# Performance work log

Hardware: AMD Instinct MI355X
Metric: run time of the kernel (lower is better)

## Reference

```python
import jax, jax.numpy as jnp
import numpy as np
from jax import lax

T, B, I, H = 512, 32, 1024, 1024


def setup_inputs() -> dict:
    key = jax.random.key(0)
    ks = jax.random.split(key, 7)
    s_i = 1.0 / np.sqrt(I)
    s_h = 1.0 / np.sqrt(H)
    return {
        "x": jax.random.normal(ks[0], (T, B, I), jnp.float32),
        "w_ih_0": jax.random.normal(ks[1], (4 * H, I), jnp.float32) * s_i,
        "w_hh_0": jax.random.normal(ks[2], (4 * H, H), jnp.float32) * s_h,
        "b_0": jax.random.normal(ks[3], (4 * H,), jnp.float32) * 0.1,
        "w_ih_1": jax.random.normal(ks[4], (4 * H, H), jnp.float32) * s_h,
        "w_hh_1": jax.random.normal(ks[5], (4 * H, H), jnp.float32) * s_h,
        "b_1": jax.random.normal(ks[6], (4 * H,), jnp.float32) * 0.1,
    }


def _sublstm_layer(inp, w_ih, w_hh, b):
    # Premultiply all timesteps at once (PremulLayer): [T,B,4H]
    pre = jnp.einsum('tbi,gi->tbg', inp, w_ih) + b
    Bsz = inp.shape[1]
    Hd = w_hh.shape[1]
    w_hh_t = w_hh.T  # [H,4H]

    def step(carry, p_t):
        h, c = carry
        gates = jax.nn.sigmoid(p_t + h @ w_hh_t)  # [B,4H]
        i_g, o_g, z_g, f_g = jnp.split(gates, 4, axis=-1)
        c = c * f_g + z_g - i_g
        h = jax.nn.sigmoid(c) - o_g
        return (h, c), h

    init = (jnp.zeros((Bsz, Hd), inp.dtype), jnp.zeros((Bsz, Hd), inp.dtype))
    _, outs = lax.scan(step, init, pre)
    return outs  # [T,B,H]


def reference(x, w_ih_0, w_hh_0, b_0, w_ih_1, w_hh_1, b_1):
    out = _sublstm_layer(x, w_ih_0, w_hh_0, b_0)
    out = _sublstm_layer(out, w_ih_1, w_hh_1, b_1)
    return out
```

## Files before the change

### kernel.cpp

```cpp
#include <hip/hip_runtime.h>
#include <hip/hip_fp16.h>
#include <stdint.h>

typedef _Float16 f16;
typedef _Float16 f16x8 __attribute__((ext_vector_type(8)));
typedef _Float16 f16x4 __attribute__((ext_vector_type(4)));
typedef float f32x4 __attribute__((ext_vector_type(4)));
typedef unsigned u32x4 __attribute__((ext_vector_type(4)));

#define TSTEPS 512
#define NB 256
#define NT 512
#define HN (32 * 1024)

__device__ __forceinline__ float sigm(float v) { return 1.0f / (1.0f + __expf(-v)); }

__device__ __forceinline__ void ld_coh(f16x8& d, const f16* p) {
  asm volatile("global_load_dwordx4 %0, %1, off sc0 sc1" : "=v"(d) : "v"(p));
}
__device__ __forceinline__ void ld_plain(f16x8& d, const f16* p) {
  asm volatile("global_load_dwordx4 %0, %1, off" : "=v"(d) : "v"(p));
}
__device__ __forceinline__ void st_coh_f16(f16* p, f16 v) {
  asm volatile("global_store_short %0, %1, off sc0 sc1" :: "v"(p), "v"(v) : "memory");
}
__device__ __forceinline__ void st_coh_u32(unsigned* p, unsigned v) {
  asm volatile("global_store_dword %0, %1, off sc0 sc1" :: "v"(p), "v"(v) : "memory");
}
__device__ __forceinline__ u32x4 ld_coh_u4(const unsigned* p) {
  u32x4 d;
  asm volatile("global_load_dwordx4 %0, %1, off sc0 sc1" : "=v"(d) : "v"(p));
  return d;
}
__device__ __forceinline__ unsigned ld_coh_u32(const unsigned* p) {
  unsigned d;
  asm volatile("global_load_dword %0, %1, off sc0 sc1" : "=v"(d) : "v"(p));
  return d;
}

template<int USE_X16>
__global__ __launch_bounds__(NT, 2)
void sublstm_persistent(const float* __restrict__ x,
                        const float* __restrict__ wih0, const float* __restrict__ whh0,
                        const float* __restrict__ b0,
                        const float* __restrict__ wih1, const float* __restrict__ whh1,
                        const float* __restrict__ b1,
                        const f16* __restrict__ x16,
                        f16* __restrict__ h1buf, f16* __restrict__ h2buf,
                        unsigned* __restrict__ bar,
                        float* __restrict__ out)
{
  __shared__ float red[8][16][68];
  __shared__ float gatesS[16][68];
  __shared__ float biasS[64];

  const int bid   = blockIdx.x;
  const int layer = bid >> 7;
  const int n     = (bid & 127) >> 1;
  const int r     = bid & 1;
  const int tid   = threadIdx.x;
  const int lane  = tid & 63;
  const int w     = tid >> 6;
  const int c15   = lane & 15;
  const int g4    = lane >> 4;
  unsigned* genp  = bar + 320;

  const float* wih = layer ? wih1 : wih0;
  const float* whh = layer ? whh1 : whh0;
  const float* bb  = layer ? b1   : b0;

  const int kbase = w * 256 + g4 * 8;
  f16x8 breg[4][8];
  #pragma unroll
  for (int cc = 0; cc < 4; ++cc) {
    const int gate = cc * 1024 + (n << 4) + c15;
    const float* wr = (w < 4) ? (wih + (size_t)gate * 1024 + kbase)
                              : (whh + (size_t)gate * 1024 + (kbase - 1024));
    #pragma unroll
    for (int ks = 0; ks < 8; ++ks) {
      const float4 v0 = *(const float4*)(wr + ks * 32);
      const float4 v1 = *(const float4*)(wr + ks * 32 + 4);
      breg[cc][ks] = (f16x8){(f16)v0.x,(f16)v0.y,(f16)v0.z,(f16)v0.w,
                             (f16)v1.x,(f16)v1.y,(f16)v1.z,(f16)v1.w};
    }
  }
  if (tid < 64) biasS[tid] = bb[(tid >> 4) * 1024 + (n << 4) + (tid & 15)];
  __syncthreads();

  float c = 0.0f;
  f16x8 af[8];
  const int arow = r * 16 + c15;

  for (int s = 0; s <= TSTEPS; ++s) {
    const int p_in  = s & 1;
    const int p_out = (s + 1) & 1;
    const bool active = (layer == 0) ? (s < TSTEPS) : (s >= 1);
    const int t = (layer == 0) ? s : (s - 1);
    const unsigned us = (unsigned)s;

    if (active && layer == 0 && w < 4) {
      if (USE_X16) {
        const f16* bp = x16 + ((size_t)t * 32 + arow) * 1024 + kbase;
        #pragma unroll
        for (int ks = 0; ks < 8; ++ks) ld_plain(af[ks], bp + ks * 32);
      } else {
        const float* bp = x + ((size_t)t * 32 + arow) * 1024 + kbase;
        #pragma unroll
        for (int ks = 0; ks < 8; ++ks) {
          const float4 v0 = *(const float4*)(bp + ks * 32);
          const float4 v1 = *(const float4*)(bp + ks * 32 + 4);
          af[ks] = (f16x8){(f16)v0.x,(f16)v0.y,(f16)v0.z,(f16)v0.w,
                           (f16)v1.x,(f16)v1.y,(f16)v1.z,(f16)v1.w};
        }
      }
    }

    if (s >= 1) {
      if (bid == 0 && w == 0) {
        while (true) {
          u32x4 d = ld_coh_u4(bar + (lane << 2));
          asm volatile("s_waitcnt vmcnt(0)" ::: "memory");
          __builtin_amdgcn_sched_barrier(0);
          if (__all(d.x >= us && d.y >= us && d.z >= us && d.w >= us)) break;
          __builtin_amdgcn_s_sleep(1);
        }
        if (lane == 0) st_coh_u32(genp, us);
      } else if (tid == 0) {
        while (true) {
          const unsigned gv = ld_coh_u32(genp);
          asm volatile("s_waitcnt vmcnt(0)" ::: "memory");
          __builtin_amdgcn_sched_barrier(0);
          if (gv >= us) break;
          __builtin_amdgcn_s_sleep(1);
        }
      }
      __syncthreads();
    }

    if (active) {
      if (!(layer == 0 && w < 4)) {
        const f16* src; int koff;
        if (layer == 0)   { src = h1buf + (size_t)p_in * HN; koff = kbase - 1024; }
        else if (w < 4)   { src = h1buf + (size_t)p_in * HN; koff = kbase; }
        else              { src = h2buf + (size_t)p_in * HN; koff = kbase - 1024; }
        const f16* bp = src + (size_t)arow * 1024 + koff;
        #pragma unroll
        for (int ks = 0; ks < 8; ++ks) ld_coh(af[ks], bp + ks * 32);
      }
      asm volatile("s_waitcnt vmcnt(0)" ::: "memory");
      __builtin_amdgcn_sched_barrier(0);

      f32x4 acc[4] = {{0,0,0,0},{0,0,0,0},{0,0,0,0},{0,0,0,0}};
      #pragma unroll
      for (int ks = 0; ks < 8; ++ks)
        #pragma unroll
        for (int cc = 0; cc < 4; ++cc)
          acc[cc] = __builtin_amdgcn_mfma_f32_16x16x32_f16(af[ks], breg[cc][ks], acc[cc], 0, 0, 0);

      #pragma unroll
      for (int cc = 0; cc < 4; ++cc)
        #pragma unroll
        for (int rr = 0; rr < 4; ++rr)
          red[w][g4 * 4 + rr][cc * 16 + c15] = acc[cc][rr];
    }
    __syncthreads();

    if (active) {
      #pragma unroll
      for (int rep = 0; rep < 2; ++rep) {
        const int idx = tid + rep * 512;
        const int lb = idx >> 6, col = idx & 63;
        float tot = biasS[col];
        #pragma unroll
        for (int ww = 0; ww < 8; ++ww) tot += red[ww][lb][col];
        gatesS[lb][col] = sigm(tot);
      }
    }
    __syncthreads();

    if (active && tid < 256) {
      const int lb = tid >> 4, u = tid & 15;
      const float ig = gatesS[lb][u];
      const float og = gatesS[lb][16 + u];
      const float zg = gatesS[lb][32 + u];
      const float fg = gatesS[lb][48 + u];
      c = c * fg + zg - ig;
      const float h = sigm(c) - og;
      const int b = r * 16 + lb;
      const int j = (n << 4) + u;
      f16* hb = ((layer == 0) ? h1buf : h2buf) + (size_t)p_out * HN;
      st_coh_f16(hb + b * 1024 + j, (f16)h);
      if (layer == 1) out[((size_t)t * 32 + b) * 1024 + j] = h;
    }

    asm volatile("s_waitcnt vmcnt(0)" ::: "memory");
    __syncthreads();
    if (tid == 0 && s < TSTEPS) st_coh_u32(bar + bid, us + 1u);
  }
}

__global__ void cvt_x_kernel(const float4* __restrict__ in, f16x4* __restrict__ outv, int n4) {
  int i = blockIdx.x * blockDim.x + threadIdx.x;
  const int stride = gridDim.x * blockDim.x;
  for (; i < n4; i += stride) {
    const float4 v = in[i];
    outv[i] = (f16x4){(f16)v.x, (f16)v.y, (f16)v.z, (f16)v.w};
  }
}

extern "C" void kernel_launch(void* const* d_in, const int* in_sizes, int n_in,
                              void* d_out, int out_size, void* d_ws, size_t ws_size,
                              hipStream_t stream) {
  const float* x    = (const float*)d_in[0];
  const float* wih0 = (const float*)d_in[1];
  const float* whh0 = (const float*)d_in[2];
  const float* b0   = (const float*)d_in[3];
  const float* wih1 = (const float*)d_in[4];
  const float* whh1 = (const float*)d_in[5];
  const float* b1   = (const float*)d_in[6];
  float* out = (float*)d_out;

  const size_t X16B   = (size_t)512 * 32 * 1024 * 2;
  const size_t HBUFB  = (size_t)2 * HN * 2;
  const size_t STATEB = 2 * HBUFB + 4096;

  char* ws = (char*)d_ws;
  const bool use_x16 = ws_size >= X16B + STATEB;
  const size_t soff = use_x16 ? X16B : 0;
  f16* x16        = (f16*)ws;
  f16* h1buf      = (f16*)(ws + soff);
  f16* h2buf      = (f16*)(ws + soff + HBUFB);
  unsigned* bar   = (unsigned*)(ws + soff + 2 * HBUFB);

  (void)hipMemsetAsync(ws + soff, 0, STATEB, stream);

  if (use_x16) {
    const int n4 = 512 * 32 * 1024 / 4;
    cvt_x_kernel<<<2048, 256, 0, stream>>>((const float4*)x, (f16x4*)x16, n4);
    sublstm_persistent<1><<<NB, NT, 0, stream>>>(x, wih0, whh0, b0, wih1, whh1, b1,
                                                 x16, h1buf, h2buf, bar, out);
  } else {
    sublstm_persistent<0><<<NB, NT, 0, stream>>>(x, wih0, whh0, b0, wih1, whh1, b1,
                                                 x16, h1buf, h2buf, bar, out);
  }
}
```

Measured before the change: 2.455 ms.

## Pad barrier flags to separate cache lines and fan out generation flags

Each block's arrival flag now sits on its own 64-byte line, and the coordinator writes 64 separate generation flags. Blocks poll these in groups, so they no longer all spin on one shared line. The hidden-state loads now go through normal caching, with an acquire fence placed after the barrier. The output stores become coherent stores. Together this aims to cut contention and latency on the global grid barrier and the h loads. The risk is correctness if the acquire fence does not invalidate stale cached h data, and the coordinator now issues four scalar loads per lane instead of one vector load.

```diff
diff --git a/kernel.cpp b/kernel.cpp
--- a/kernel.cpp
+++ b/kernel.cpp
@@ -15,22 +15,17 @@
 
 __device__ __forceinline__ float sigm(float v) { return 1.0f / (1.0f + __expf(-v)); }
 
-__device__ __forceinline__ void ld_coh(f16x8& d, const f16* p) {
-  asm volatile("global_load_dwordx4 %0, %1, off sc0 sc1" : "=v"(d) : "v"(p));
-}
 __device__ __forceinline__ void ld_plain(f16x8& d, const f16* p) {
   asm volatile("global_load_dwordx4 %0, %1, off" : "=v"(d) : "v"(p));
 }
 __device__ __forceinline__ void st_coh_f16(f16* p, f16 v) {
   asm volatile("global_store_short %0, %1, off sc0 sc1" :: "v"(p), "v"(v) : "memory");
 }
+__device__ __forceinline__ void st_coh_f32(float* p, float v) {
+  asm volatile("global_store_dword %0, %1, off sc0 sc1" :: "v"(p), "v"(v) : "memory");
+}
 __device__ __forceinline__ void st_coh_u32(unsigned* p, unsigned v) {
   asm volatile("global_store_dword %0, %1, off sc0 sc1" :: "v"(p), "v"(v) : "memory");
-}
-__device__ __forceinline__ u32x4 ld_coh_u4(const unsigned* p) {
-  u32x4 d;
-  asm volatile("global_load_dwordx4 %0, %1, off sc0 sc1" : "=v"(d) : "v"(p));
-  return d;
 }
 __device__ __forceinline__ unsigned ld_coh_u32(const unsigned* p) {
   unsigned d;
@@ -63,7 +58,6 @@
   const int w     = tid >> 6;
   const int c15   = lane & 15;
   const int g4    = lane >> 4;
-  unsigned* genp  = bar + 320;
 
   const float* wih = layer ? wih1 : wih0;
   const float* whh = layer ? whh1 : whh0;
@@ -118,16 +112,20 @@
     if (s >= 1) {
       if (bid == 0 && w == 0) {
         while (true) {
-          u32x4 d = ld_coh_u4(bar + (lane << 2));
+          const unsigned f0 = ld_coh_u32(bar + (lane * 4 + 0) * 16);
+          const unsigned f1 = ld_coh_u32(bar + (lane * 4 + 1) * 16);
+          const unsigned f2 = ld_coh_u32(bar + (lane * 4 + 2) * 16);
+          const unsigned f3 = ld_coh_u32(bar + (lane * 4 + 3) * 16);
           asm volatile("s_waitcnt vmcnt(0)" ::: "memory");
           __builtin_amdgcn_sched_barrier(0);
-          if (__all(d.x >= us && d.y >= us && d.z >= us && d.w >= us)) break;
+          if (__all(f0 >= us && f1 >= us && f2 >= us && f3 >= us)) break;
           __builtin_amdgcn_s_sleep(1);
         }
-        if (lane == 0) st_coh_u32(genp, us);
+        st_coh_u32(bar + 4096 + lane * 16, us);
       } else if (tid == 0) {
+        const unsigned* gp = bar + 4096 + (bid & 63) * 16;
         while (true) {
-          const unsigned gv = ld_coh_u32(genp);
+          const unsigned gv = ld_coh_u32(gp);
           asm volatile("s_waitcnt vmcnt(0)" ::: "memory");
           __builtin_amdgcn_sched_barrier(0);
           if (gv >= us) break;
@@ -135,6 +133,7 @@
         }
       }
       __syncthreads();
+      __builtin_amdgcn_fence(__ATOMIC_ACQUIRE, "agent");
     }
 
     if (active) {
@@ -145,7 +144,7 @@
         else              { src = h2buf + (size_t)p_in * HN; koff = kbase - 1024; }
         const f16* bp = src + (size_t)arow * 1024 + koff;
         #pragma unroll
-        for (int ks = 0; ks < 8; ++ks) ld_coh(af[ks], bp + ks * 32);
+        for (int ks = 0; ks < 8; ++ks) ld_plain(af[ks], bp + ks * 32);
       }
       asm volatile("s_waitcnt vmcnt(0)" ::: "memory");
       __builtin_amdgcn_sched_barrier(0);
@@ -190,12 +189,12 @@
       const int j = (n << 4) + u;
       f16* hb = ((layer == 0) ? h1buf : h2buf) + (size_t)p_out * HN;
       st_coh_f16(hb + b * 1024 + j, (f16)h);
-      if (layer == 1) out[((size_t)t * 32 + b) * 1024 + j] = h;
+      if (layer == 1) st_coh_f32(out + ((size_t)t * 32 + b) * 1024 + j, h);
     }
 
     asm volatile("s_waitcnt vmcnt(0)" ::: "memory");
     __syncthreads();
-    if (tid == 0 && s < TSTEPS) st_coh_u32(bar + bid, us + 1u);
+    if (tid == 0 && s < TSTEPS) st_coh_u32(bar + bid * 16, us + 1u);
   }
 }
 
@@ -222,7 +221,8 @@
 
   const size_t X16B   = (size_t)512 * 32 * 1024 * 2;
   const size_t HBUFB  = (size_t)2 * HN * 2;
-  const size_t STATEB = 2 * HBUFB + 4096;
+  const size_t BARB   = 32768;
+  const size_t STATEB = 2 * HBUFB + BARB;
 
   char* ws = (char*)d_ws;
   const bool use_x16 = ws_size >= X16B + STATEB;
```

Measured after the change: 9.641 ms. +292.7%, slower.

## Tag hidden-state words with step counters to replace the global barrier wait

Applied to the files above, without the earlier changes.

Each hidden value is now stored as a 32-bit word holding the fp16 value plus a step tag in the upper half. Consumers spin on their own input slices until every tag matches the expected step, instead of waiting for the centralized generation barrier before loading. The remaining generation-barrier wait, which still guards against overwriting the double buffer, is moved after the gate computation. The goal is to take the global barrier round trip off the critical path. In exchange the hidden-state loads are twice as wide, each poll spins on several vector loads, and buffer reuse safety now depends on the later barrier.

```diff
diff --git a/kernel.cpp b/kernel.cpp
--- a/kernel.cpp
+++ b/kernel.cpp
@@ -15,14 +15,8 @@
 
 __device__ __forceinline__ float sigm(float v) { return 1.0f / (1.0f + __expf(-v)); }
 
-__device__ __forceinline__ void ld_coh(f16x8& d, const f16* p) {
-  asm volatile("global_load_dwordx4 %0, %1, off sc0 sc1" : "=v"(d) : "v"(p));
-}
 __device__ __forceinline__ void ld_plain(f16x8& d, const f16* p) {
   asm volatile("global_load_dwordx4 %0, %1, off" : "=v"(d) : "v"(p));
-}
-__device__ __forceinline__ void st_coh_f16(f16* p, f16 v) {
-  asm volatile("global_store_short %0, %1, off sc0 sc1" :: "v"(p), "v"(v) : "memory");
 }
 __device__ __forceinline__ void st_coh_u32(unsigned* p, unsigned v) {
   asm volatile("global_store_dword %0, %1, off sc0 sc1" :: "v"(p), "v"(v) : "memory");
@@ -46,7 +40,7 @@
                         const float* __restrict__ wih1, const float* __restrict__ whh1,
                         const float* __restrict__ b1,
                         const f16* __restrict__ x16,
-                        f16* __restrict__ h1buf, f16* __restrict__ h2buf,
+                        unsigned* __restrict__ h1u, unsigned* __restrict__ h2u,
                         unsigned* __restrict__ bar,
                         float* __restrict__ out)
 {
@@ -115,17 +109,85 @@
       }
     }
 
-    if (s >= 1) {
-      if (bid == 0 && w == 0) {
+    if (s >= 1 && bid == 0 && w == 0) {
+      while (true) {
+        u32x4 d = ld_coh_u4(bar + (lane << 2));
+        asm volatile("s_waitcnt vmcnt(0)" ::: "memory");
+        __builtin_amdgcn_sched_barrier(0);
+        if (__all(d.x >= us && d.y >= us && d.z >= us && d.w >= us)) break;
+        __builtin_amdgcn_s_sleep(1);
+      }
+      if (lane == 0) st_coh_u32(genp, us);
+    }
+
+    if (active) {
+      if (!(layer == 0 && w < 4)) {
+        const unsigned* srcU; int koff; unsigned expv;
+        if (layer == 0)   { srcU = h1u + (size_t)p_in * HN; koff = kbase - 1024; expv = us; }
+        else if (w < 4)   { srcU = h1u + (size_t)p_in * HN; koff = kbase;        expv = us; }
+        else              { srcU = h2u + (size_t)p_in * HN; koff = kbase - 1024; expv = (s == 1) ? 0u : us; }
+        const unsigned* bp = srcU + (size_t)arow * 1024 + koff;
+        const unsigned expw = expv << 16;
+        u32x4 t0[8], t1[8];
         while (true) {
-          u32x4 d = ld_coh_u4(bar + (lane << 2));
+          #pragma unroll
+          for (int ks = 0; ks < 8; ++ks) {
+            t0[ks] = ld_coh_u4(bp + ks * 32);
+            t1[ks] = ld_coh_u4(bp + ks * 32 + 4);
+          }
           asm volatile("s_waitcnt vmcnt(0)" ::: "memory");
           __builtin_amdgcn_sched_barrier(0);
-          if (__all(d.x >= us && d.y >= us && d.z >= us && d.w >= us)) break;
+          unsigned bad = 0;
+          #pragma unroll
+          for (int ks = 0; ks < 8; ++ks) {
+            bad |= (t0[ks].x ^ expw) | (t0[ks].y ^ expw) | (t0[ks].z ^ expw) | (t0[ks].w ^ expw)
+                 | (t1[ks].x ^ expw) | (t1[ks].y ^ expw) | (t1[ks].z ^ expw) | (t1[ks].w ^ expw);
+          }
+          if (!__any((bad & 0xffff0000u) != 0u)) break;
           __builtin_amdgcn_s_sleep(1);
         }
-        if (lane == 0) st_coh_u32(genp, us);
-      } else if (tid == 0) {
+        #pragma unroll
+        for (int ks = 0; ks < 8; ++ks) {
+          const unsigned w0 = (t0[ks].x & 0xffffu) | (t0[ks].y << 16);
+          const unsigned w1 = (t0[ks].z & 0xffffu) | (t0[ks].w << 16);
+          const unsigned w2 = (t1[ks].x & 0xffffu) | (t1[ks].y << 16);
+          const unsigned w3 = (t1[ks].z & 0xffffu) | (t1[ks].w << 16);
+          af[ks] = __builtin_bit_cast(f16x8, (u32x4){w0, w1, w2, w3});
+        }
+      }
+      asm volatile("s_waitcnt vmcnt(0)" ::: "memory");
+      __builtin_amdgcn_sched_barrier(0);
+
+      f32x4 acc[4] = {{0,0,0,0},{0,0,0,0},{0,0,0,0},{0,0,0,0}};
+      #pragma unroll
+      for (int ks = 0; ks < 8; ++ks)
+        #pragma unroll
+        for (int cc = 0; cc < 4; ++cc)
+          acc[cc] = __builtin_amdgcn_mfma_f32_16x16x32_f16(af[ks], breg[cc][ks], acc[cc], 0, 0, 0);
+
+      #pragma unroll
+      for (int cc = 0; cc < 4; ++cc)
+        #pragma unroll
+        for (int rr = 0; rr < 4; ++rr)
+          red[w][g4 * 4 + rr][cc * 16 + c15] = acc[cc][rr];
+    }
+    __syncthreads();
+
+    if (active) {
+      #pragma unroll
+      for (int rep = 0; rep < 2; ++rep) {
+        const int idx = tid + rep * 512;
+        const int lb = idx >> 6, col = idx & 63;
+        float tot = biasS[col];
+        #pragma unroll
+        for (int ww = 0; ww < 8; ++ww) tot += red[ww][lb][col];
+        gatesS[lb][col] = sigm(tot);
+      }
+    }
+    __syncthreads();
+
+    if (active && s >= 1) {
+      if (tid == 0) {
         while (true) {
           const unsigned gv = ld_coh_u32(genp);
           asm volatile("s_waitcnt vmcnt(0)" ::: "memory");
@@ -136,47 +198,6 @@
       }
       __syncthreads();
     }
-
-    if (active) {
-      if (!(layer == 0 && w < 4)) {
-        const f16* src; int koff;
-        if (layer == 0)   { src = h1buf + (size_t)p_in * HN; koff = kbase - 1024; }
-        else if (w < 4)   { src = h1buf + (size_t)p_in * HN; koff = kbase; }
-        else              { src = h2buf + (size_t)p_in * HN; koff = kbase - 1024; }
-        const f16* bp = src + (size_t)arow * 1024 + koff;
-        #pragma unroll
-        for (int ks = 0; ks < 8; ++ks) ld_coh(af[ks], bp + ks * 32);
-      }
-      asm volatile("s_waitcnt vmcnt(0)" ::: "memory");
-      __builtin_amdgcn_sched_barrier(0);
-
-      f32x4 acc[4] = {{0,0,0,0},{0,0,0,0},{0,0,0,0},{0,0,0,0}};
-      #pragma unroll
-      for (int ks = 0; ks < 8; ++ks)
-        #pragma unroll
-        for (int cc = 0; cc < 4; ++cc)
-          acc[cc] = __builtin_amdgcn_mfma_f32_16x16x32_f16(af[ks], breg[cc][ks], acc[cc], 0, 0, 0);
-
-      #pragma unroll
-      for (int cc = 0; cc < 4; ++cc)
-        #pragma unroll
-        for (int rr = 0; rr < 4; ++rr)
-          red[w][g4 * 4 + rr][cc * 16 + c15] = acc[cc][rr];
-    }
-    __syncthreads();
-
-    if (active) {
-      #pragma unroll
-      for (int rep = 0; rep < 2; ++rep) {
-        const int idx = tid + rep * 512;
-        const int lb = idx >> 6, col = idx & 63;
-        float tot = biasS[col];
-        #pragma unroll
-        for (int ww = 0; ww < 8; ++ww) tot += red[ww][lb][col];
-        gatesS[lb][col] = sigm(tot);
-      }
-    }
-    __syncthreads();
 
     if (active && tid < 256) {
       const int lb = tid >> 4, u = tid & 15;
@@ -188,8 +209,10 @@
       const float h = sigm(c) - og;
       const int b = r * 16 + lb;
       const int j = (n << 4) + u;
-      f16* hb = ((layer == 0) ? h1buf : h2buf) + (size_t)p_out * HN;
-      st_coh_f16(hb + b * 1024 + j, (f16)h);
+      unsigned* hb = ((layer == 0) ? h1u : h2u) + (size_t)p_out * HN;
+      const unsigned hv = ((unsigned)(s + 1) << 16) |
+                          (unsigned)__builtin_bit_cast(unsigned short, (f16)h);
+      st_coh_u32(hb + b * 1024 + j, hv);
       if (layer == 1) out[((size_t)t * 32 + b) * 1024 + j] = h;
     }
 
@@ -221,15 +244,15 @@
   float* out = (float*)d_out;
 
   const size_t X16B   = (size_t)512 * 32 * 1024 * 2;
-  const size_t HBUFB  = (size_t)2 * HN * 2;
+  const size_t HBUFB  = (size_t)2 * HN * 4;
   const size_t STATEB = 2 * HBUFB + 4096;
 
   char* ws = (char*)d_ws;
   const bool use_x16 = ws_size >= X16B + STATEB;
   const size_t soff = use_x16 ? X16B : 0;
   f16* x16        = (f16*)ws;
-  f16* h1buf      = (f16*)(ws + soff);
-  f16* h2buf      = (f16*)(ws + soff + HBUFB);
+  unsigned* h1u   = (unsigned*)(ws + soff);
+  unsigned* h2u   = (unsigned*)(ws + soff + HBUFB);
   unsigned* bar   = (unsigned*)(ws + soff + 2 * HBUFB);
 
   (void)hipMemsetAsync(ws + soff, 0, STATEB, stream);
@@ -238,9 +261,9 @@
     const int n4 = 512 * 32 * 1024 / 4;
     cvt_x_kernel<<<2048, 256, 0, stream>>>((const float4*)x, (f16x4*)x16, n4);
     sublstm_persistent<1><<<NB, NT, 0, stream>>>(x, wih0, whh0, b0, wih1, whh1, b1,
-                                                 x16, h1buf, h2buf, bar, out);
+                                                 x16, h1u, h2u, bar, out);
   } else {
     sublstm_persistent<0><<<NB, NT, 0, stream>>>(x, wih0, whh0, b0, wih1, whh1, b1,
-                                                 x16, h1buf, h2buf, bar, out);
-  }
-}
+                                                 x16, h1u, h2u, bar, out);
+  }
+}
```

Result: slower. 2.840 ms (+15.7%).

## Coalesce h loads via swizzled LDS staging and vectorize h stores

Applied to the files above, without the earlier changes.

Each wave now loads its hidden-state slice with row-contiguous 512-byte coalesced reads, writes it to a XOR-swizzled LDS stage, and reads back the MFMA A-fragment layout from LDS. The h output is gathered into shared memory and written as 16-byte coherent stores instead of per-element 2-byte stores. This is meant to cut the number and scatter of coherent global transactions on the per-step critical path. In exchange it adds 64KB of LDS per block, an extra LDS round trip and an additional __syncthreads each step, which could hurt occupancy at 2 blocks per CU.

```diff
diff --git a/kernel.cpp b/kernel.cpp
--- a/kernel.cpp
+++ b/kernel.cpp
@@ -21,8 +21,8 @@
 __device__ __forceinline__ void ld_plain(f16x8& d, const f16* p) {
   asm volatile("global_load_dwordx4 %0, %1, off" : "=v"(d) : "v"(p));
 }
-__device__ __forceinline__ void st_coh_f16(f16* p, f16 v) {
-  asm volatile("global_store_short %0, %1, off sc0 sc1" :: "v"(p), "v"(v) : "memory");
+__device__ __forceinline__ void st_coh_f16x8(f16* p, f16x8 v) {
+  asm volatile("global_store_dwordx4 %0, %1, off sc0 sc1" :: "v"(p), "v"(v) : "memory");
 }
 __device__ __forceinline__ void st_coh_u32(unsigned* p, unsigned v) {
   asm volatile("global_store_dword %0, %1, off sc0 sc1" :: "v"(p), "v"(v) : "memory");
@@ -53,6 +53,8 @@
   __shared__ float red[8][16][68];
   __shared__ float gatesS[16][68];
   __shared__ float biasS[64];
+  __shared__ f16 stage[8][4096];
+  __shared__ f16 hstageS[16][16];
 
   const int bid   = blockIdx.x;
   const int layer = bid >> 7;
@@ -63,6 +65,8 @@
   const int w     = tid >> 6;
   const int c15   = lane & 15;
   const int g4    = lane >> 4;
+  const int l5    = lane & 31;
+  const int lh    = lane >> 5;
   unsigned* genp  = bar + 320;
 
   const float* wih = layer ? wih1 : wih0;
@@ -139,13 +143,33 @@
 
     if (active) {
       if (!(layer == 0 && w < 4)) {
-        const f16* src; int koff;
-        if (layer == 0)   { src = h1buf + (size_t)p_in * HN; koff = kbase - 1024; }
-        else if (w < 4)   { src = h1buf + (size_t)p_in * HN; koff = kbase; }
-        else              { src = h2buf + (size_t)p_in * HN; koff = kbase - 1024; }
-        const f16* bp = src + (size_t)arow * 1024 + koff;
-        #pragma unroll
-        for (int ks = 0; ks < 8; ++ks) ld_coh(af[ks], bp + ks * 32);
+        const f16* src; int kslice;
+        if (layer == 0)   { src = h1buf + (size_t)p_in * HN; kslice = w * 256 - 1024; }
+        else if (w < 4)   { src = h1buf + (size_t)p_in * HN; kslice = w * 256; }
+        else              { src = h2buf + (size_t)p_in * HN; kslice = w * 256 - 1024; }
+        #pragma unroll
+        for (int i = 0; i < 8; ++i) {
+          const int row = 2 * i + lh;
+          ld_coh(af[i], src + (size_t)(r * 16 + row) * 1024 + kslice + l5 * 8);
+        }
+        asm volatile("s_waitcnt vmcnt(0)" ::: "memory");
+        __builtin_amdgcn_sched_barrier(0);
+        char* st = (char*)&stage[w][0];
+        #pragma unroll
+        for (int i = 0; i < 8; ++i) {
+          const int row = 2 * i + lh;
+          const unsigned byte = ((unsigned)row << 9) |
+                                ((((unsigned)l5 ^ ((unsigned)row & 7u)) << 4));
+          *(f16x8*)(st + byte) = af[i];
+        }
+        asm volatile("s_waitcnt lgkmcnt(0)" ::: "memory");
+        __builtin_amdgcn_sched_barrier(0);
+        #pragma unroll
+        for (int ks = 0; ks < 8; ++ks) {
+          const unsigned chunk = ((unsigned)(4 * ks + g4)) ^ ((unsigned)c15 & 7u);
+          const unsigned byte = ((unsigned)c15 << 9) | (chunk << 4);
+          af[ks] = *(const f16x8*)(st + byte);
+        }
       }
       asm volatile("s_waitcnt vmcnt(0)" ::: "memory");
       __builtin_amdgcn_sched_barrier(0);
@@ -186,11 +210,17 @@
       const float fg = gatesS[lb][48 + u];
       c = c * fg + zg - ig;
       const float h = sigm(c) - og;
+      hstageS[lb][u] = (f16)h;
       const int b = r * 16 + lb;
-      const int j = (n << 4) + u;
+      if (layer == 1) out[((size_t)t * 32 + b) * 1024 + (n << 4) + u] = h;
+    }
+    __syncthreads();
+
+    if (active && w == 0 && lane < 32) {
+      const int row = lane >> 1, half = lane & 1;
+      f16x8 v = *(const f16x8*)&hstageS[row][half * 8];
       f16* hb = ((layer == 0) ? h1buf : h2buf) + (size_t)p_out * HN;
-      st_coh_f16(hb + b * 1024 + j, (f16)h);
-      if (layer == 1) out[((size_t)t * 32 + b) * 1024 + j] = h;
+      st_coh_f16x8(hb + (size_t)(r * 16 + row) * 1024 + (n << 4) + half * 8, v);
     }
 
     asm volatile("s_waitcnt vmcnt(0)" ::: "memory");
```

Measured after the change: 2.220 ms. -9.5%, faster.
